# Optimization experiments

Measured on AMD Instinct MI355X. Metric: run time of the kernel, lower is better.

## Reference

```python
import jax, jax.numpy as jnp
import numpy as np

N_NODES = 50000
N_EDGES = 800000
N_GRAPHS = 128
HEADS = 4
HDIM = 32
N_CLASSES = 10
LEAKY_ALPHA = 0.2


def setup_inputs() -> dict:
    key = jax.random.key(0)
    ks = jax.random.split(key, 12)
    src = jax.random.randint(ks[0], (N_EDGES,), 0, N_NODES, dtype=jnp.int32)
    # guarantee every node has in-degree >= 1 so 3/deg is finite
    dst_tail = jax.random.randint(ks[1], (N_EDGES - N_NODES,), 0, N_NODES, dtype=jnp.int32)
    dst = jnp.concatenate([jnp.arange(N_NODES, dtype=jnp.int32), dst_tail])
    graph_ids = jnp.sort(jax.random.randint(ks[2], (N_NODES,), 0, N_GRAPHS, dtype=jnp.int32))
    s = 0.1
    return {
        "src": src,
        "dst": dst,
        "graph_ids": graph_ids,
        "W1": jax.random.normal(ks[3], (4, HEADS * HDIM), jnp.float32) * s,
        "al1": jax.random.normal(ks[4], (HEADS, HDIM), jnp.float32) * s,
        "ar1": jax.random.normal(ks[5], (HEADS, HDIM), jnp.float32) * s,
        "W2": jax.random.normal(ks[6], (HEADS * HDIM, HEADS * HDIM), jnp.float32) * s,
        "al2": jax.random.normal(ks[7], (HEADS, HDIM), jnp.float32) * s,
        "ar2": jax.random.normal(ks[8], (HEADS, HDIM), jnp.float32) * s,
        "Wc": jax.random.normal(ks[9], (HEADS * HDIM, N_CLASSES), jnp.float32) * s,
        "bc": jax.random.normal(ks[10], (N_CLASSES,), jnp.float32) * s,
    }


def _gat_layer(x, src, dst, W, al, ar):
    # x: [N, Fin]; W: [Fin, H*D]; al, ar: [H, D]
    n = x.shape[0]
    ft = (x @ W).reshape(n, HEADS, HDIM)                       # [N, H, D]
    a1 = jnp.einsum("nhd,hd->nh", ft, al)                      # [N, H]
    a2 = jnp.einsum("nhd,hd->nh", ft, ar)                      # [N, H]
    e = jax.nn.leaky_relu(a1[src] + a2[dst], LEAKY_ALPHA)      # [E, H]
    # segment softmax over incoming edges of each dst node
    m = jax.ops.segment_max(e, dst, num_segments=n)            # [N, H]
    m = jax.lax.stop_gradient(m)
    ex = jnp.exp(e - m[dst])                                   # [E, H]
    denom = jax.ops.segment_sum(ex, dst, num_segments=n)       # [N, H]
    alpha = ex / denom[dst]                                    # [E, H]
    # gather-multiply-scatter aggregation
    out = jax.ops.segment_sum(ft[src] * alpha[:, :, None], dst, num_segments=n)  # [N, H, D]
    return jax.nn.relu(out.reshape(n, HEADS * HDIM))


def reference(src, dst, graph_ids, W1, al1, ar1, W2, al2, ar2, Wc, bc):
    n = N_NODES
    ones_e = jnp.ones(src.shape[0], jnp.float32)
    deg = jax.ops.segment_sum(ones_e, dst, num_segments=n)     # in-degrees [N]
    h = jnp.stack(
        [deg, (deg - 3.0 > 0).astype(jnp.float32), 3.0 / deg, (deg - 4.0 > 0).astype(jnp.float32)],
        axis=1,
    )                                                          # [N, 4]
    h = _gat_layer(h, src, dst, W1, al1, ar1)                  # [N, H*D]
    h = _gat_layer(h, src, dst, W2, al2, ar2)                  # [N, H*D]
    # mean_nodes: per-graph mean pooling
    gsum = jax.ops.segment_sum(h, graph_ids, num_segments=N_GRAPHS)
    cnt = jax.ops.segment_sum(jnp.ones(n, jnp.float32), graph_ids, num_segments=N_GRAPHS)
    gmean = gsum / jnp.maximum(cnt, 1.0)[:, None]              # [G, H*D]
    return jax.nn.sigmoid(gmean @ Wc + bc)                     # [G, n_classes]
```

## Files before the change

kernel.cpp:

```cpp
#include <hip/hip_runtime.h>
#include <hip/hip_fp16.h>
#include <math.h>

#define HEADS 4
#define HDIM 32
#define FDIM 128
#define NGRAPH 128
#define NCLASS 10

#define NBW 128
#define NBP 512
#define BCAP 4096
#define SLICE 4096

typedef _Float16 h4_t __attribute__((ext_vector_type(4)));
typedef float f4_t __attribute__((ext_vector_type(4)));
typedef float f2_t __attribute__((ext_vector_type(2)));

__device__ __forceinline__ float lrelu(float x) { return fmaxf(x, 0.2f * x); }

__global__ void k_wfrag(const float* __restrict__ W2, __half* __restrict__ Wfrag,
                        float* __restrict__ gsum, int* __restrict__ gcnt,
                        int* __restrict__ bcur) {
    int gid = blockIdx.x * 256 + threadIdx.x;
    ((float4*)gsum)[gid] = make_float4(0.f, 0.f, 0.f, 0.f);
    if (gid < NGRAPH) gcnt[gid] = 0;
    if (gid < NBP) bcur[gid] = 0;
    int fid = gid >> 6, l = gid & 63;
    int ks = fid >> 3, t = fid & 7;
    int k0 = ks * 16 + 4 * (l >> 4);
    int n0 = t * 16 + (l & 15);
    __half2 lo = __floats2half2_rn(W2[(k0 + 0) * FDIM + n0], W2[(k0 + 1) * FDIM + n0]);
    __half2 hi = __floats2half2_rn(W2[(k0 + 2) * FDIM + n0], W2[(k0 + 3) * FDIM + n0]);
    size_t base = ((size_t)fid * 64 + l) * 4;
    *(__half2*)(Wfrag + base)     = lo;
    *(__half2*)(Wfrag + base + 2) = hi;
}

__global__ __launch_bounds__(256) void k_part(const int* __restrict__ src,
        const int* __restrict__ dst, int E, int* __restrict__ bcur,
        unsigned int* __restrict__ part) {
    __shared__ int lcnt[NBP];
    __shared__ int loff[NBP];
    __shared__ int lpos[NBP];
    __shared__ unsigned int staged[SLICE];
    __shared__ int tgt[SLICE];
    __shared__ int ws[4];
    int tid = threadIdx.x, lane = tid & 63, w = tid >> 6;
    int beg = blockIdx.x * SLICE, end = min(E, beg + SLICE);
    int m = end - beg;
    for (int i = tid; i < NBP; i += 256) lcnt[i] = 0;
    __syncthreads();
    for (int i = beg + tid; i < end; i += 256)
        atomicAdd(&lcnt[dst[i] >> 7], 1);
    __syncthreads();
    int c0 = lcnt[2 * tid], c1 = lcnt[2 * tid + 1];
    int t = c0 + c1;
    int incl = t;
    #pragma unroll
    for (int off = 1; off < 64; off <<= 1) {
        int y = __shfl_up(incl, off);
        if (lane >= off) incl += y;
    }
    if (lane == 63) ws[w] = incl;
    __syncthreads();
    int wpre = 0;
    #pragma unroll
    for (int j = 0; j < 4; ++j) if (j < w) wpre += ws[j];
    int ex = wpre + (incl - t);
    loff[2 * tid] = ex; loff[2 * tid + 1] = ex + c0;
    if (c0) lpos[2 * tid] = atomicAdd(&bcur[2 * tid], c0);
    if (c1) lpos[2 * tid + 1] = atomicAdd(&bcur[2 * tid + 1], c1);
    lcnt[2 * tid] = 0; lcnt[2 * tid + 1] = 0;
    __syncthreads();
    for (int i = beg + tid; i < end; i += 256) {
        int s = src[i], d = dst[i];
        int b = d >> 7;
        int idx = atomicAdd(&lcnt[b], 1);
        int slot = loff[b] + idx;
        staged[slot] = ((unsigned int)(d & (NBW - 1)) << 16) | (unsigned int)s;
        tgt[slot] = b * BCAP + lpos[b] + idx;
    }
    __syncthreads();
    for (int i = tid; i < m; i += 256)
        part[tgt[i]] = staged[i];
}

__global__ __launch_bounds__(256) void k_build(const unsigned int* __restrict__ part,
        const int* __restrict__ bcur, const float* __restrict__ W1,
        const float* __restrict__ al, const float* __restrict__ ar,
        unsigned int* __restrict__ nodeinfo, unsigned short* __restrict__ csr,
        float* __restrict__ h4t, float* __restrict__ a1, float* __restrict__ a2, int n) {
    __shared__ int ldeg[NBW];
    __shared__ int loffs[NBW];
    __shared__ int wtot[2];
    __shared__ float wla[16], wlr[16];
    int b = blockIdx.x, tid = threadIdx.x;
    int lane = tid & 63, w = tid >> 6;
    if (tid < NBW) ldeg[tid] = 0;
    if (tid < 32) {
        int k = (tid & 15) >> 2, h = tid & 3;
        const float* av = (tid < 16) ? al : ar;
        float s = 0.f;
        #pragma unroll
        for (int d = 0; d < 32; ++d) s += W1[k * FDIM + h * HDIM + d] * av[h * HDIM + d];
        if (tid < 16) wla[k * 4 + h] = s; else wlr[k * 4 + h] = s;
    }
    __syncthreads();
    int beg = b * BCAP, end = beg + bcur[b];
    for (int i = beg + tid; i < end; i += 256)
        atomicAdd(&ldeg[part[i] >> 16], 1);
    __syncthreads();
    int x = (tid < NBW) ? ldeg[tid] : 0;
    int incl = x;
    #pragma unroll
    for (int off = 1; off < 64; off <<= 1) {
        int y = __shfl_up(incl, off);
        if (lane >= off) incl += y;
    }
    if (tid < NBW && lane == 63) wtot[w] = incl;
    __syncthreads();
    if (tid < NBW) {
        int pre = incl - x;
        if (w == 1) pre += wtot[0];
        loffs[tid] = beg + pre;
        int v = b * NBW + tid;
        if (v < n) {
            nodeinfo[v] = ((unsigned int)(beg + pre) << 9) | (unsigned int)x;
            float d = (float)x;
            float4 hv = make_float4(d, (d - 3.0f > 0.0f) ? 1.0f : 0.0f, 3.0f / d,
                                    (d - 4.0f > 0.0f) ? 1.0f : 0.0f);
            *(float4*)(h4t + v * 4) = hv;
            float4 o1, o2;
            #pragma unroll
            for (int h = 0; h < 4; ++h) {
                float s1 = hv.x * wla[0 + h] + hv.y * wla[4 + h] + hv.z * wla[8 + h] + hv.w * wla[12 + h];
                float s2 = hv.x * wlr[0 + h] + hv.y * wlr[4 + h] + hv.z * wlr[8 + h] + hv.w * wlr[12 + h];
                if (h == 0) { o1.x = s1; o2.x = s2; } else if (h == 1) { o1.y = s1; o2.y = s2; }
                else if (h == 2) { o1.z = s1; o2.z = s2; } else { o1.w = s1; o2.w = s2; }
            }
            *(float4*)(a1 + v * 4) = o1;
            *(float4*)(a2 + v * 4) = o2;
        }
    }
    __syncthreads();
    if (tid < NBW) ldeg[tid] = 0;
    __syncthreads();
    for (int i = beg + tid; i < end; i += 256) {
        unsigned int e = part[i];
        int lv = e >> 16;
        int p = atomicAdd(&ldeg[lv], 1);
        csr[loffs[lv] + p] = (unsigned short)(e & 0xffffu);
    }
}

__global__ __launch_bounds__(256) void k_l2f(const unsigned int* __restrict__ nodeinfo,
        const unsigned short* __restrict__ csr, const float* __restrict__ h4t,
        const float* __restrict__ a1, const float* __restrict__ a2,
        const float* __restrict__ W1, const __half* __restrict__ Wfrag,
        const float* __restrict__ al, const float* __restrict__ ar,
        unsigned char* __restrict__ ft8, float* __restrict__ a1b,
        float* __restrict__ a2b, int n) {
    __shared__ __half Blds[64 * 64 * 4];
    __shared__ __half Alds[4][16 * 132];
    __shared__ float Slds[4][256];
    int tid = threadIdx.x, l = tid & 63, w = tid >> 6;
    int c = l & 15, g = l >> 4;

    #pragma unroll
    for (int i = 0; i < 8; ++i)
        ((float4*)Blds)[i * 256 + tid] = ((const float4*)Wfrag)[i * 256 + tid];

    int v0 = (blockIdx.x * 4 + w) * 16;

    for (int r4 = 0; r4 < 4; ++r4) {
        int v = v0 + r4 * 4 + g;
        bool vok = v < n;
        unsigned int info = vok ? nodeinfo[v] : 0;
        int beg = info >> 9;
        int dg = info & 511;
        float4 a2v = vok ? *(const float4*)(a2 + v * 4) : make_float4(0, 0, 0, 0);
        float P[4][4], D[4];
        #pragma unroll
        for (int h = 0; h < 4; ++h) { D[h] = 0.f;
            #pragma unroll
            for (int d = 0; d < 4; ++d) P[h][d] = 0.f; }
        for (int base2 = 0; base2 < dg; base2 += 16) {
            if (base2 + c < dg) {
                int u = csr[beg + base2 + c];
                float4 a1u = *(const float4*)(a1 + u * 4);
                float4 f4  = *(const float4*)(h4t + u * 4);
                float wgt[4];
                wgt[0] = __expf(lrelu(a1u.x + a2v.x));
                wgt[1] = __expf(lrelu(a1u.y + a2v.y));
                wgt[2] = __expf(lrelu(a1u.z + a2v.z));
                wgt[3] = __expf(lrelu(a1u.w + a2v.w));
                #pragma unroll
                for (int h = 0; h < 4; ++h) {
                    D[h] += wgt[h];
                    P[h][0] = fmaf(wgt[h], f4.x, P[h][0]);
                    P[h][1] = fmaf(wgt[h], f4.y, P[h][1]);
                    P[h][2] = fmaf(wgt[h], f4.z, P[h][2]);
                    P[h][3] = fmaf(wgt[h], f4.w, P[h][3]);
                }
            }
        }
        #pragma unroll
        for (int off = 1; off < 16; off <<= 1) {
            #pragma unroll
            for (int h = 0; h < 4; ++h) {
                D[h] += __shfl_xor(D[h], off);
                #pragma unroll
                for (int d = 0; d < 4; ++d) P[h][d] += __shfl_xor(P[h][d], off);
            }
        }
        if (vok && c == 0) {
            #pragma unroll
            for (int h = 0; h < 4; ++h) {
                float r = 1.0f / D[h];
                #pragma unroll
                for (int d = 0; d < 4; ++d)
                    Slds[w][(r4 * 4 + g) * 16 + h * 4 + d] = P[h][d] * r;
            }
        }
    }

    float2 w1c[4];
    #pragma unroll
    for (int d = 0; d < 4; ++d) w1c[d] = *(const float2*)(W1 + d * FDIM + 2 * l);
    for (int jj = 0; jj < 16; ++jj) {
        float4 s = *(const float4*)(&Slds[w][jj * 16 + g * 4]);
        float t0 = s.x * w1c[0].x + s.y * w1c[1].x + s.z * w1c[2].x + s.w * w1c[3].x;
        float t1 = s.x * w1c[0].y + s.y * w1c[1].y + s.z * w1c[2].y + s.w * w1c[3].y;
        *(__half2*)(&Alds[w][jj * 132 + 2 * l]) = __floats2half2_rn(fmaxf(t0, 0.f), fmaxf(t1, 0.f));
    }
    __syncthreads();

    f4_t acc[8];
    #pragma unroll
    for (int t = 0; t < 8; ++t) acc[t] = (f4_t){0.f, 0.f, 0.f, 0.f};
    #pragma unroll
    for (int ks = 0; ks < 8; ++ks) {
        h4_t af = *(const h4_t*)(&Alds[w][c * 132 + ks * 16 + 4 * g]);
        #pragma unroll
        for (int t = 0; t < 8; ++t) {
            h4_t bf = *(const h4_t*)(&Blds[((ks * 8 + t) * 64 + l) * 4]);
            acc[t] = __builtin_amdgcn_mfma_f32_16x16x16f16(af, bf, acc[t], 0, 0, 0);
        }
    }

    #pragma unroll
    for (int t = 0; t < 8; ++t) {
        #pragma unroll
        for (int r = 0; r < 4; ++r) {
            int v = v0 + 4 * g + r;
            if (v < n) {
                int pk = __builtin_amdgcn_cvt_pk_fp8_f32(acc[t][r], acc[t][r], 0, false);
                ft8[(size_t)v * FDIM + t * 16 + c] = (unsigned char)(pk & 0xff);
            }
        }
    }
    float al0[4], al1v[4], ar0[4], ar1v[4];
    #pragma unroll
    for (int h = 0; h < 4; ++h) {
        al0[h] = al[h * 32 + c]; al1v[h] = al[h * 32 + 16 + c];
        ar0[h] = ar[h * 32 + c]; ar1v[h] = ar[h * 32 + 16 + c];
    }
    #pragma unroll
    for (int r = 0; r < 4; ++r) {
        int v = v0 + 4 * g + r;
        #pragma unroll
        for (int h = 0; h < 4; ++h) {
            float p1 = acc[2 * h][r] * al0[h] + acc[2 * h + 1][r] * al1v[h];
            float p2 = acc[2 * h][r] * ar0[h] + acc[2 * h + 1][r] * ar1v[h];
            #pragma unroll
            for (int off = 1; off < 16; off <<= 1) {
                p1 += __shfl_xor(p1, off);
                p2 += __shfl_xor(p2, off);
            }
            if (c == h && v < n) {
                a1b[v * 4 + h] = p1;
                a2b[v * 4 + h] = p2;
            }
        }
    }
}

__global__ __launch_bounds__(256) void k_agg2(const unsigned int* __restrict__ nodeinfo,
        const unsigned short* __restrict__ csr, const unsigned char* __restrict__ ft8,
        const float* __restrict__ a1, const float* __restrict__ a2,
        __half* __restrict__ out, int n) {
    int tid = threadIdx.x, lane = tid & 63, w = tid >> 6;
    int qw = lane >> 4, ql = lane & 15;
    int v = blockIdx.x * 16 + w * 4 + qw;
    if (v >= n) return;
    unsigned int info = nodeinfo[v];
    int beg = info >> 9, end = beg + (info & 511);
    int h = ql >> 2;
    float a2h = a2[v * 4 + h];
    float acc[8];
    #pragma unroll
    for (int k = 0; k < 8; ++k) acc[k] = 0.f;
    float dsum = 0.f;
    const unsigned char* fbase = ft8 + (size_t)ql * 8;
    int j = beg;
    for (; j + 2 <= end; j += 2) {
        int s0 = csr[j], s1 = csr[j + 1];
        float w0 = __expf(lrelu(a1[s0 * 4 + h] + a2h));
        float w1 = __expf(lrelu(a1[s1 * 4 + h] + a2h));
        uint2 b0 = *(const uint2*)(fbase + (size_t)s0 * FDIM);
        uint2 b1 = *(const uint2*)(fbase + (size_t)s1 * FDIM);
        dsum += w0 + w1;
        f2_t g;
        g = __builtin_amdgcn_cvt_pk_f32_fp8(b0.x, false); acc[0] = fmaf(w0, g[0], acc[0]); acc[1] = fmaf(w0, g[1], acc[1]);
        g = __builtin_amdgcn_cvt_pk_f32_fp8(b0.x, true);  acc[2] = fmaf(w0, g[0], acc[2]); acc[3] = fmaf(w0, g[1], acc[3]);
        g = __builtin_amdgcn_cvt_pk_f32_fp8(b0.y, false); acc[4] = fmaf(w0, g[0], acc[4]); acc[5] = fmaf(w0, g[1], acc[5]);
        g = __builtin_amdgcn_cvt_pk_f32_fp8(b0.y, true);  acc[6] = fmaf(w0, g[0], acc[6]); acc[7] = fmaf(w0, g[1], acc[7]);
        g = __builtin_amdgcn_cvt_pk_f32_fp8(b1.x, false); acc[0] = fmaf(w1, g[0], acc[0]); acc[1] = fmaf(w1, g[1], acc[1]);
        g = __builtin_amdgcn_cvt_pk_f32_fp8(b1.x, true);  acc[2] = fmaf(w1, g[0], acc[2]); acc[3] = fmaf(w1, g[1], acc[3]);
        g = __builtin_amdgcn_cvt_pk_f32_fp8(b1.y, false); acc[4] = fmaf(w1, g[0], acc[4]); acc[5] = fmaf(w1, g[1], acc[5]);
        g = __builtin_amdgcn_cvt_pk_f32_fp8(b1.y, true);  acc[6] = fmaf(w1, g[0], acc[6]); acc[7] = fmaf(w1, g[1], acc[7]);
    }
    for (; j < end; ++j) {
        int s0 = csr[j];
        float w0 = __expf(lrelu(a1[s0 * 4 + h] + a2h));
        uint2 b0 = *(const uint2*)(fbase + (size_t)s0 * FDIM);
        dsum += w0;
        f2_t g;
        g = __builtin_amdgcn_cvt_pk_f32_fp8(b0.x, false); acc[0] = fmaf(w0, g[0], acc[0]); acc[1] = fmaf(w0, g[1], acc[1]);
        g = __builtin_amdgcn_cvt_pk_f32_fp8(b0.x, true);  acc[2] = fmaf(w0, g[0], acc[2]); acc[3] = fmaf(w0, g[1], acc[3]);
        g = __builtin_amdgcn_cvt_pk_f32_fp8(b0.y, false); acc[4] = fmaf(w0, g[0], acc[4]); acc[5] = fmaf(w0, g[1], acc[5]);
        g = __builtin_amdgcn_cvt_pk_f32_fp8(b0.y, true);  acc[6] = fmaf(w0, g[0], acc[6]); acc[7] = fmaf(w0, g[1], acc[7]);
    }
    float r = 1.0f / dsum;
    __half2 o[4];
    #pragma unroll
    for (int k = 0; k < 4; ++k)
        o[k] = __floats2half2_rn(fmaxf(acc[2 * k] * r, 0.f), fmaxf(acc[2 * k + 1] * r, 0.f));
    *(float4*)(out + (size_t)v * FDIM + ql * 8) = *(float4*)o;
}

__global__ void k_pool(const __half* __restrict__ hbuf, const int* __restrict__ gid,
                       float* __restrict__ gsum, int* __restrict__ gcnt, int n) {
    const int STRIP = 32;
    int wv = (blockIdx.x * blockDim.x + threadIdx.x) >> 6;
    int lane = threadIdx.x & 63;
    int beg = wv * STRIP;
    if (beg >= n) return;
    int end = min(beg + STRIP, n);
    int f = 2 * lane;
    float2 acc = make_float2(0.f, 0.f);
    int cur = gid[beg];
    int cnt = 0;
    for (int i = beg; i < end; ++i) {
        int g = gid[i];
        if (g != cur) {
            atomicAdd(&gsum[cur * FDIM + f], acc.x);
            atomicAdd(&gsum[cur * FDIM + f + 1], acc.y);
            if (lane == 0) atomicAdd(&gcnt[cur], cnt);
            acc = make_float2(0.f, 0.f); cnt = 0; cur = g;
        }
        float2 x = __half22float2(*(const __half2*)(hbuf + (size_t)i * FDIM + f));
        acc.x += x.x; acc.y += x.y; cnt++;
    }
    atomicAdd(&gsum[cur * FDIM + f], acc.x);
    atomicAdd(&gsum[cur * FDIM + f + 1], acc.y);
    if (lane == 0) atomicAdd(&gcnt[cur], cnt);
}

__global__ void k_classify(const float* __restrict__ gsum, const int* __restrict__ gcnt,
                           const float* __restrict__ Wc, const float* __restrict__ bc,
                           float* __restrict__ out) {
    int idx = blockIdx.x * blockDim.x + threadIdx.x;
    if (idx >= NGRAPH * NCLASS) return;
    int g = idx / NCLASS, c = idx % NCLASS;
    float rc = 1.0f / fmaxf((float)gcnt[g], 1.0f);
    float s = bc[c];
    for (int k = 0; k < FDIM; ++k)
        s += gsum[g * FDIM + k] * rc * Wc[k * NCLASS + c];
    out[idx] = 1.0f / (1.0f + __expf(-s));
}

extern "C" void kernel_launch(void* const* d_in, const int* in_sizes, int n_in,
                              void* d_out, int out_size, void* d_ws, size_t ws_size,
                              hipStream_t stream) {
    const int*   src = (const int*)d_in[0];
    const int*   dst = (const int*)d_in[1];
    const int*   gid = (const int*)d_in[2];
    const float* W1  = (const float*)d_in[3];
    const float* al1 = (const float*)d_in[4];
    const float* ar1 = (const float*)d_in[5];
    const float* W2  = (const float*)d_in[6];
    const float* al2 = (const float*)d_in[7];
    const float* ar2 = (const float*)d_in[8];
    const float* Wc  = (const float*)d_in[9];
    const float* bc  = (const float*)d_in[10];
    float* out = (float*)d_out;
    const int E = in_sizes[0];
    const int N = in_sizes[2];

    char* ws = (char*)d_ws;
    size_t off = 0;
    auto alloc = [&](size_t bytes) -> void* {
        void* p = ws + off;
        off = (off + bytes + 255) & ~(size_t)255;
        return p;
    };
    unsigned int*   part = (unsigned int*)alloc((size_t)NBP * BCAP * 4);
    unsigned short* csr  = (unsigned short*)alloc((size_t)NBP * BCAP * 2);
    int*    bcur   = (int*)alloc(NBP * 4);
    unsigned int* nodeinfo = (unsigned int*)alloc((size_t)N * 4);
    float*  h4t    = (float*)alloc((size_t)N * 4 * 4);
    float*  a1     = (float*)alloc((size_t)N * HEADS * 4);
    float*  a2     = (float*)alloc((size_t)N * HEADS * 4);
    float*  a1b    = (float*)alloc((size_t)N * HEADS * 4);
    float*  a2b    = (float*)alloc((size_t)N * HEADS * 4);
    unsigned char* ft8 = (unsigned char*)alloc((size_t)N * FDIM);
    __half* hbuf   = (__half*)alloc((size_t)N * FDIM * 2);
    __half* Wfrag  = (__half*)alloc((size_t)FDIM * FDIM * 2);
    float*  gsum   = (float*)alloc((size_t)NGRAPH * FDIM * 4);
    int*    gcnt   = (int*)alloc((size_t)NGRAPH * 4);

    int pb_edges = (E + SLICE - 1) / SLICE;
    int nb2 = (N + NBW - 1) / NBW;

    k_wfrag<<<16, 256, 0, stream>>>(W2, Wfrag, gsum, gcnt, bcur);
    k_part<<<pb_edges, 256, 0, stream>>>(src, dst, E, bcur, part);
    k_build<<<nb2, 256, 0, stream>>>(part, bcur, W1, al1, ar1,
                                     nodeinfo, csr, h4t, a1, a2, N);
    k_l2f<<<(N + 63) / 64, 256, 0, stream>>>(nodeinfo, csr, h4t, a1, a2, W1, Wfrag,
                                             al2, ar2, ft8, a1b, a2b, N);
    k_agg2<<<(N + 15) / 16, 256, 0, stream>>>(nodeinfo, csr, ft8, a1b, a2b, hbuf, N);

    int pb = (((N + 31) / 32) + 3) / 4;
    k_pool<<<pb, 256, 0, stream>>>(hbuf, gid, gsum, gcnt, N);
    k_classify<<<(NGRAPH * NCLASS + 255) / 256, 256, 0, stream>>>(gsum, gcnt, Wc, bc, out);
}
```

Measured before the change: 122.0 us.

## Recompute layer-1 features from 16-bit degrees and unroll layer-2 gather by four

The build kernel now writes only a 16-bit in-degree per node instead of the 4-float feature vector and two 4-float attention-logit arrays. The layer-1 aggregation rebuilds the features and attention logits on the fly from the neighbour's degree using precomputed W1·al/ar weights in shared memory. This swaps 48 bytes of gathered data per edge for 2 bytes plus a few FMAs and a divide. Separately, the layer-2 aggregation loop is unrolled from 2 to 4 edges, which raises the number of gathers in flight per thread.

```diff
diff --git a/kernel.cpp b/kernel.cpp
--- a/kernel.cpp
+++ b/kernel.cpp
@@ -87,25 +87,14 @@
 }
 
 __global__ __launch_bounds__(256) void k_build(const unsigned int* __restrict__ part,
-        const int* __restrict__ bcur, const float* __restrict__ W1,
-        const float* __restrict__ al, const float* __restrict__ ar,
-        unsigned int* __restrict__ nodeinfo, unsigned short* __restrict__ csr,
-        float* __restrict__ h4t, float* __restrict__ a1, float* __restrict__ a2, int n) {
+        const int* __restrict__ bcur, unsigned int* __restrict__ nodeinfo,
+        unsigned short* __restrict__ csr, unsigned short* __restrict__ deg16, int n) {
     __shared__ int ldeg[NBW];
     __shared__ int loffs[NBW];
     __shared__ int wtot[2];
-    __shared__ float wla[16], wlr[16];
     int b = blockIdx.x, tid = threadIdx.x;
     int lane = tid & 63, w = tid >> 6;
     if (tid < NBW) ldeg[tid] = 0;
-    if (tid < 32) {
-        int k = (tid & 15) >> 2, h = tid & 3;
-        const float* av = (tid < 16) ? al : ar;
-        float s = 0.f;
-        #pragma unroll
-        for (int d = 0; d < 32; ++d) s += W1[k * FDIM + h * HDIM + d] * av[h * HDIM + d];
-        if (tid < 16) wla[k * 4 + h] = s; else wlr[k * 4 + h] = s;
-    }
     __syncthreads();
     int beg = b * BCAP, end = beg + bcur[b];
     for (int i = beg + tid; i < end; i += 256)
@@ -127,20 +116,7 @@
         int v = b * NBW + tid;
         if (v < n) {
             nodeinfo[v] = ((unsigned int)(beg + pre) << 9) | (unsigned int)x;
-            float d = (float)x;
-            float4 hv = make_float4(d, (d - 3.0f > 0.0f) ? 1.0f : 0.0f, 3.0f / d,
-                                    (d - 4.0f > 0.0f) ? 1.0f : 0.0f);
-            *(float4*)(h4t + v * 4) = hv;
-            float4 o1, o2;
-            #pragma unroll
-            for (int h = 0; h < 4; ++h) {
-                float s1 = hv.x * wla[0 + h] + hv.y * wla[4 + h] + hv.z * wla[8 + h] + hv.w * wla[12 + h];
-                float s2 = hv.x * wlr[0 + h] + hv.y * wlr[4 + h] + hv.z * wlr[8 + h] + hv.w * wlr[12 + h];
-                if (h == 0) { o1.x = s1; o2.x = s2; } else if (h == 1) { o1.y = s1; o2.y = s2; }
-                else if (h == 2) { o1.z = s1; o2.z = s2; } else { o1.w = s1; o2.w = s2; }
-            }
-            *(float4*)(a1 + v * 4) = o1;
-            *(float4*)(a2 + v * 4) = o2;
+            deg16[v] = (unsigned short)x;
         }
     }
     __syncthreads();
@@ -155,21 +131,31 @@
 }
 
 __global__ __launch_bounds__(256) void k_l2f(const unsigned int* __restrict__ nodeinfo,
-        const unsigned short* __restrict__ csr, const float* __restrict__ h4t,
-        const float* __restrict__ a1, const float* __restrict__ a2,
-        const float* __restrict__ W1, const __half* __restrict__ Wfrag,
+        const unsigned short* __restrict__ csr, const unsigned short* __restrict__ deg16,
+        const float* __restrict__ W1, const float* __restrict__ al1,
+        const float* __restrict__ ar1, const __half* __restrict__ Wfrag,
         const float* __restrict__ al, const float* __restrict__ ar,
         unsigned char* __restrict__ ft8, float* __restrict__ a1b,
         float* __restrict__ a2b, int n) {
     __shared__ __half Blds[64 * 64 * 4];
     __shared__ __half Alds[4][16 * 132];
     __shared__ float Slds[4][256];
+    __shared__ float wla[16], wlr[16];
     int tid = threadIdx.x, l = tid & 63, w = tid >> 6;
     int c = l & 15, g = l >> 4;
 
+    if (tid < 32) {
+        int k = (tid & 15) >> 2, h = tid & 3;
+        const float* av = (tid < 16) ? al1 : ar1;
+        float s = 0.f;
+        #pragma unroll
+        for (int d = 0; d < 32; ++d) s += W1[k * FDIM + h * HDIM + d] * av[h * HDIM + d];
+        if (tid < 16) wla[k * 4 + h] = s; else wlr[k * 4 + h] = s;
+    }
     #pragma unroll
     for (int i = 0; i < 8; ++i)
         ((float4*)Blds)[i * 256 + tid] = ((const float4*)Wfrag)[i * 256 + tid];
+    __syncthreads();
 
     int v0 = (blockIdx.x * 4 + w) * 16;
 
@@ -179,7 +165,13 @@
         unsigned int info = vok ? nodeinfo[v] : 0;
         int beg = info >> 9;
         int dg = info & 511;
-        float4 a2v = vok ? *(const float4*)(a2 + v * 4) : make_float4(0, 0, 0, 0);
+        float dv = vok ? (float)dg : 1.0f;
+        float4 hvv = make_float4(dv, (dv - 3.0f > 0.0f) ? 1.0f : 0.0f, 3.0f / dv,
+                                 (dv - 4.0f > 0.0f) ? 1.0f : 0.0f);
+        float a2h[4];
+        #pragma unroll
+        for (int h = 0; h < 4; ++h)
+            a2h[h] = hvv.x * wlr[0 + h] + hvv.y * wlr[4 + h] + hvv.z * wlr[8 + h] + hvv.w * wlr[12 + h];
         float P[4][4], D[4];
         #pragma unroll
         for (int h = 0; h < 4; ++h) { D[h] = 0.f;
@@ -188,20 +180,22 @@
         for (int base2 = 0; base2 < dg; base2 += 16) {
             if (base2 + c < dg) {
                 int u = csr[beg + base2 + c];
-                float4 a1u = *(const float4*)(a1 + u * 4);
-                float4 f4  = *(const float4*)(h4t + u * 4);
+                float du = (float)deg16[u];
+                float4 fu = make_float4(du, (du - 3.0f > 0.0f) ? 1.0f : 0.0f, 3.0f / du,
+                                        (du - 4.0f > 0.0f) ? 1.0f : 0.0f);
                 float wgt[4];
-                wgt[0] = __expf(lrelu(a1u.x + a2v.x));
-                wgt[1] = __expf(lrelu(a1u.y + a2v.y));
-                wgt[2] = __expf(lrelu(a1u.z + a2v.z));
-                wgt[3] = __expf(lrelu(a1u.w + a2v.w));
+                #pragma unroll
+                for (int h = 0; h < 4; ++h) {
+                    float a1h = fu.x * wla[0 + h] + fu.y * wla[4 + h] + fu.z * wla[8 + h] + fu.w * wla[12 + h];
+                    wgt[h] = __expf(lrelu(a1h + a2h[h]));
+                }
                 #pragma unroll
                 for (int h = 0; h < 4; ++h) {
                     D[h] += wgt[h];
-                    P[h][0] = fmaf(wgt[h], f4.x, P[h][0]);
-                    P[h][1] = fmaf(wgt[h], f4.y, P[h][1]);
-                    P[h][2] = fmaf(wgt[h], f4.z, P[h][2]);
-                    P[h][3] = fmaf(wgt[h], f4.w, P[h][3]);
+                    P[h][0] = fmaf(wgt[h], fu.x, P[h][0]);
+                    P[h][1] = fmaf(wgt[h], fu.y, P[h][1]);
+                    P[h][2] = fmaf(wgt[h], fu.z, P[h][2]);
+                    P[h][3] = fmaf(wgt[h], fu.w, P[h][3]);
                 }
             }
         }
@@ -304,22 +298,25 @@
     float dsum = 0.f;
     const unsigned char* fbase = ft8 + (size_t)ql * 8;
     int j = beg;
-    for (; j + 2 <= end; j += 2) {
-        int s0 = csr[j], s1 = csr[j + 1];
-        float w0 = __expf(lrelu(a1[s0 * 4 + h] + a2h));
-        float w1 = __expf(lrelu(a1[s1 * 4 + h] + a2h));
-        uint2 b0 = *(const uint2*)(fbase + (size_t)s0 * FDIM);
-        uint2 b1 = *(const uint2*)(fbase + (size_t)s1 * FDIM);
-        dsum += w0 + w1;
-        f2_t g;
-        g = __builtin_amdgcn_cvt_pk_f32_fp8(b0.x, false); acc[0] = fmaf(w0, g[0], acc[0]); acc[1] = fmaf(w0, g[1], acc[1]);
-        g = __builtin_amdgcn_cvt_pk_f32_fp8(b0.x, true);  acc[2] = fmaf(w0, g[0], acc[2]); acc[3] = fmaf(w0, g[1], acc[3]);
-        g = __builtin_amdgcn_cvt_pk_f32_fp8(b0.y, false); acc[4] = fmaf(w0, g[0], acc[4]); acc[5] = fmaf(w0, g[1], acc[5]);
-        g = __builtin_amdgcn_cvt_pk_f32_fp8(b0.y, true);  acc[6] = fmaf(w0, g[0], acc[6]); acc[7] = fmaf(w0, g[1], acc[7]);
-        g = __builtin_amdgcn_cvt_pk_f32_fp8(b1.x, false); acc[0] = fmaf(w1, g[0], acc[0]); acc[1] = fmaf(w1, g[1], acc[1]);
-        g = __builtin_amdgcn_cvt_pk_f32_fp8(b1.x, true);  acc[2] = fmaf(w1, g[0], acc[2]); acc[3] = fmaf(w1, g[1], acc[3]);
-        g = __builtin_amdgcn_cvt_pk_f32_fp8(b1.y, false); acc[4] = fmaf(w1, g[0], acc[4]); acc[5] = fmaf(w1, g[1], acc[5]);
-        g = __builtin_amdgcn_cvt_pk_f32_fp8(b1.y, true);  acc[6] = fmaf(w1, g[0], acc[6]); acc[7] = fmaf(w1, g[1], acc[7]);
+    for (; j + 4 <= end; j += 4) {
+        int s[4];
+        #pragma unroll
+        for (int k = 0; k < 4; ++k) s[k] = csr[j + k];
+        float wv[4]; uint2 bv[4];
+        #pragma unroll
+        for (int k = 0; k < 4; ++k) {
+            wv[k] = __expf(lrelu(a1[s[k] * 4 + h] + a2h));
+            bv[k] = *(const uint2*)(fbase + (size_t)s[k] * FDIM);
+        }
+        #pragma unroll
+        for (int k = 0; k < 4; ++k) {
+            dsum += wv[k];
+            f2_t g;
+            g = __builtin_amdgcn_cvt_pk_f32_fp8(bv[k].x, false); acc[0] = fmaf(wv[k], g[0], acc[0]); acc[1] = fmaf(wv[k], g[1], acc[1]);
+            g = __builtin_amdgcn_cvt_pk_f32_fp8(bv[k].x, true);  acc[2] = fmaf(wv[k], g[0], acc[2]); acc[3] = fmaf(wv[k], g[1], acc[3]);
+            g = __builtin_amdgcn_cvt_pk_f32_fp8(bv[k].y, false); acc[4] = fmaf(wv[k], g[0], acc[4]); acc[5] = fmaf(wv[k], g[1], acc[5]);
+            g = __builtin_amdgcn_cvt_pk_f32_fp8(bv[k].y, true);  acc[6] = fmaf(wv[k], g[0], acc[6]); acc[7] = fmaf(wv[k], g[1], acc[7]);
+        }
     }
     for (; j < end; ++j) {
         int s0 = csr[j];
@@ -410,9 +407,7 @@
     unsigned short* csr  = (unsigned short*)alloc((size_t)NBP * BCAP * 2);
     int*    bcur   = (int*)alloc(NBP * 4);
     unsigned int* nodeinfo = (unsigned int*)alloc((size_t)N * 4);
-    float*  h4t    = (float*)alloc((size_t)N * 4 * 4);
-    float*  a1     = (float*)alloc((size_t)N * HEADS * 4);
-    float*  a2     = (float*)alloc((size_t)N * HEADS * 4);
+    unsigned short* deg16  = (unsigned short*)alloc((size_t)N * 2);
     float*  a1b    = (float*)alloc((size_t)N * HEADS * 4);
     float*  a2b    = (float*)alloc((size_t)N * HEADS * 4);
     unsigned char* ft8 = (unsigned char*)alloc((size_t)N * FDIM);
@@ -426,10 +421,9 @@
 
     k_wfrag<<<16, 256, 0, stream>>>(W2, Wfrag, gsum, gcnt, bcur);
     k_part<<<pb_edges, 256, 0, stream>>>(src, dst, E, bcur, part);
-    k_build<<<nb2, 256, 0, stream>>>(part, bcur, W1, al1, ar1,
-                                     nodeinfo, csr, h4t, a1, a2, N);
-    k_l2f<<<(N + 63) / 64, 256, 0, stream>>>(nodeinfo, csr, h4t, a1, a2, W1, Wfrag,
-                                             al2, ar2, ft8, a1b, a2b, N);
+    k_build<<<nb2, 256, 0, stream>>>(part, bcur, nodeinfo, csr, deg16, N);
+    k_l2f<<<(N + 63) / 64, 256, 0, stream>>>(nodeinfo, csr, deg16, W1, al1, ar1,
+                                             Wfrag, al2, ar2, ft8, a1b, a2b, N);
     k_agg2<<<(N + 15) / 16, 256, 0, stream>>>(nodeinfo, csr, ft8, a1b, a2b, hbuf, N);
 
     int pb = (((N + 31) / 32) + 3) / 4;
```

Result: no change. 122.1 us (+0.1%).
